# Performance work log

Measured on AMD Instinct MI355X. Metric: run time of the kernel, lower is better.

The kernel has to match this reference:

```python
import jax, jax.numpy as jnp
import numpy as np

B = 16384          # batch_size
NF = 50            # n_fields
K = 16             # embedding_dim
V = 1_000_000      # input_dim (vocab)
H = 400            # fc hidden
NNZ = B * NF


def _xavier(key, shape):
    fan_in, fan_out = shape
    lim = (6.0 / (fan_in + fan_out)) ** 0.5
    return jax.random.uniform(key, shape, minval=-lim, maxval=lim, dtype=jnp.float32)


def setup_inputs() -> dict:
    key = jax.random.key(0)
    ks = jax.random.split(key, 12)
    feats = jax.random.randint(ks[0], (NNZ,), 0, V)
    # n_fields contiguous features per sample (required by view(batch_size,-1))
    index = jnp.repeat(jnp.arange(B), NF)
    values = jax.random.uniform(ks[1], (NNZ,), dtype=jnp.float32)
    bias = jnp.zeros((1, 1), jnp.float32)
    weights = _xavier(ks[2], (V, 1))
    embedding = _xavier(ks[3], (V, K))
    d = NF * K  # 800
    W0 = _xavier(ks[4], (d, H))
    b0 = jax.random.normal(ks[5], (1, 1), jnp.float32)
    W1 = _xavier(ks[6], (H, H))
    b1 = jax.random.normal(ks[7], (1, 1), jnp.float32)
    W2 = _xavier(ks[8], (H, 1))
    b2 = jax.random.normal(ks[9], (1, 1), jnp.float32)
    return dict(index=index, feats=feats, values=values, bias=bias,
                weights=weights, embedding=embedding,
                W0=W0, b0=b0, W1=W1, b1=b1, W2=W2, b2=b2, batch_size=B)


def reference(index, feats, values, bias, weights, embedding,
              W0, b0, W1, b1, W2, b2, batch_size):
    # gather (F.embedding)
    w = weights[feats, 0]              # [nnz]
    emb = embedding[feats]             # [nnz, K]

    # first order: segment-sum of w*v, plus bias ([B] + [1,1] -> [1,B], as in torch)
    first = jax.ops.segment_sum(w * values, index, num_segments=batch_size) + bias

    # second order: FM pooling trick, fused over all K dims in one segment reduce
    ev = emb * values[:, None]                                        # [nnz, K]
    s1 = jax.ops.segment_sum(ev, index, num_segments=batch_size)      # [B, K]
    s2 = jax.ops.segment_sum(ev * ev, index, num_segments=batch_size) # [B, K]
    second = 0.5 * jnp.sum(s1 * s1 - s2, axis=1)                      # [B]

    # higher order MLP (relu on every layer, scalar biases)
    x = emb.reshape(batch_size, -1)    # [B, NF*K]
    x = jax.nn.relu(x @ W0 + b0)
    x = jax.nn.relu(x @ W1 + b1)
    x = jax.nn.relu(x @ W2 + b2)       # [B, 1]
    higher = x.reshape(-1)             # [B]

    return jax.nn.sigmoid(first + second + higher)  # [1, B]
```

## Files before the change

kernel.cpp:

```cpp
#include <hip/hip_runtime.h>
#include <hip/hip_bf16.h>


#define BATCH 16384
#define NFLD  50
#define EK    16
#define DDIM  800
#define HDIM  400
#define HPAD  416
#define NPAD  512

#define TB_W0 400
#define TB_W1 208
#define TBLK  (TB_W0 + TB_W1)
#define GBLK  (BATCH / 16)

typedef __attribute__((ext_vector_type(8))) __bf16 bf16x8;
typedef __attribute__((ext_vector_type(4))) float  f32x4;

typedef const __attribute__((address_space(1))) unsigned int* gas_u32p;
typedef __attribute__((address_space(3))) unsigned int*       las_u32p;

__device__ __forceinline__ void gld_lds16(const void* g, void* l) {
    __builtin_amdgcn_global_load_lds((gas_u32p)g, (las_u32p)l, 16, 0, 0);
}

__global__ __launch_bounds__(256) void prep_kernel(
    const float* __restrict__ W0, const float* __restrict__ W1,
    __hip_bfloat16* __restrict__ W0t, __hip_bfloat16* __restrict__ W1t,
    const int* __restrict__ feats, const float* __restrict__ values,
    const float* __restrict__ biasp, const float* __restrict__ weights,
    const float* __restrict__ embedding,
    float* __restrict__ fs, __hip_bfloat16* __restrict__ x)
{
    const int bid = blockIdx.x;
    if (bid < TBLK) {
        const int which = bid >= TB_W0;
        const int i  = which ? bid - TB_W0 : bid;
        const int nx = which ? 13 : 25;
        const int bx = i % nx, by = i / nx;
        const float* src = which ? W1 : W0;
        __hip_bfloat16* dst = which ? W1t : W0t;
        const int srcK = which ? HDIM : DDIM;
        const int dstCols = which ? HPAD : DDIM;

        __shared__ float tile[32][33];
        const int tx = threadIdx.x & 31, ty = threadIdx.x >> 5;
        const int k0 = bx * 32, n0 = by * 32;
#pragma unroll
        for (int r = 0; r < 4; ++r) {
            int k = k0 + ty + r * 8;
            int n = n0 + tx;
            float v = (k < srcK && n < HDIM) ? src[(long)k * HDIM + n] : 0.f;
            tile[ty + r * 8][tx] = v;
        }
        __syncthreads();
#pragma unroll
        for (int r = 0; r < 4; ++r) {
            int n = n0 + ty + r * 8;
            int k = k0 + tx;
            if (k < dstCols)
                dst[(long)n * dstCols + k] = __float2bfloat16(tile[tx][ty + r * 8]);
        }
        return;
    }

    const int wave = threadIdx.x >> 6;
    const int lane = threadIdx.x & 63;
    const int r    = lane >> 2, c = lane & 3;
    const int sbase = (bid - TBLK) * 16 + wave * 4;

    int   f[4] = {0, 0, 0, 0};
    float v[4] = {0.f, 0.f, 0.f, 0.f};
    float wsum[4] = {0.f, 0.f, 0.f, 0.f};
#pragma unroll
    for (int q = 0; q < 4; ++q) {
        const long base = (long)(sbase + q) * NFLD;
        if (lane < NFLD) {
            f[q] = feats[base + lane];
            v[q] = values[base + lane];
            wsum[q] = weights[f[q]] * v[q];
        }
    }

    int   fj[4][4]; float vj[4][4];
#pragma unroll
    for (int q = 0; q < 4; ++q)
#pragma unroll
        for (int p = 0; p < 4; ++p) {
            const int j = p * 16 + r;
            if (p < 3 || r < 2) {
                fj[q][p] = __shfl(f[q], j);
                vj[q][p] = __shfl(v[q], j);
            }
        }
    float4 e[4][4];
#pragma unroll
    for (int q = 0; q < 4; ++q)
#pragma unroll
        for (int p = 0; p < 4; ++p)
            if (p < 3 || r < 2)
                e[q][p] = *(const float4*)(embedding + (long)fj[q][p] * EK + c * 4);

#pragma unroll
    for (int q = 0; q < 4; ++q) {
        const int s = sbase + q;
        f32x4 s1 = {0.f, 0.f, 0.f, 0.f}, s2 = {0.f, 0.f, 0.f, 0.f};
#pragma unroll
        for (int p = 0; p < 4; ++p) {
            const int j = p * 16 + r;
            if (p < 3 || r < 2) {
                f32x4 ef = {e[q][p].x, e[q][p].y, e[q][p].z, e[q][p].w};
                f32x4 ev = ef * vj[q][p];
                s1 += ev;
                s2 += ev * ev;
                __hip_bfloat16 pk[4] = {
                    __float2bfloat16(e[q][p].x), __float2bfloat16(e[q][p].y),
                    __float2bfloat16(e[q][p].z), __float2bfloat16(e[q][p].w)};
                *(uint2*)&x[(long)s * DDIM + j * EK + c * 4] = *(uint2*)pk;
            }
        }
#pragma unroll
        for (int m = 4; m <= 32; m <<= 1) {
            s1.x += __shfl_xor(s1.x, m); s1.y += __shfl_xor(s1.y, m);
            s1.z += __shfl_xor(s1.z, m); s1.w += __shfl_xor(s1.w, m);
            s2.x += __shfl_xor(s2.x, m); s2.y += __shfl_xor(s2.y, m);
            s2.z += __shfl_xor(s2.z, m); s2.w += __shfl_xor(s2.w, m);
        }
        float t = (s1.x * s1.x - s2.x) + (s1.y * s1.y - s2.y)
                + (s1.z * s1.z - s2.z) + (s1.w * s1.w - s2.w);
        t += __shfl_xor(t, 1); t += __shfl_xor(t, 2);
        float w = wsum[q];
        w += __shfl_xor(w, 1);  w += __shfl_xor(w, 2);
        w += __shfl_xor(w, 4);  w += __shfl_xor(w, 8);
        w += __shfl_xor(w, 16); w += __shfl_xor(w, 32);
        if (lane == 0) fs[s] = w + 0.5f * t + biasp[0];
    }
}

#define OSTRIDE 136
template <int KDIM, int MODE, int LDC>
__global__ __launch_bounds__(256) void gemm_relu_kernel(
    const __hip_bfloat16* __restrict__ A,
    const __hip_bfloat16* __restrict__ Bt,
    const float* __restrict__ biasp,
    const float* __restrict__ W2,
    void* __restrict__ C)
{
    constexpr int KT = KDIM / 32;
    __shared__ __align__(16) char lds[128 * OSTRIDE * 2];
    __hip_bfloat16* sA = (__hip_bfloat16*)lds;
    __hip_bfloat16* sB = sA + 2 * 4096;
    __hip_bfloat16* sO = (__hip_bfloat16*)lds;

    const int tid  = threadIdx.x;
    const int wave = tid >> 6, lane = tid & 63;
    const int l16  = lane & 15, quad = lane >> 4;
    const int waveM = wave & 1, waveN = wave >> 1;
    const int m0 = blockIdx.y * 128;
    const int n0 = blockIdx.x * 128;

    f32x4 acc[4][4] = {};

    const long ar0 = (long)(m0 + wave * 16 + (lane >> 2)) * KDIM;
    const long ar1 = ar0 + (long)64 * KDIM;
    const long br0 = (long)(n0 + wave * 16 + (lane >> 2)) * KDIM;
    const long br1 = br0 + (long)64 * KDIM;
    const int  ac  = (lane & 3) * 8;
    __hip_bfloat16* ldsA0 = sA + wave * 512 + lane * 8;
    __hip_bfloat16* ldsA1 = sA + 2048 + wave * 512 + lane * 8;
    __hip_bfloat16* ldsB0 = sB + wave * 512 + lane * 8;
    __hip_bfloat16* ldsB1 = sB + 2048 + wave * 512 + lane * 8;

    auto stage = [&](int plane, int h) {
        const int k0 = plane * 32;
        gld_lds16(A  + ar0 + k0 + ac, ldsA0 + h * 4096);
        gld_lds16(A  + ar1 + k0 + ac, ldsA1 + h * 4096);
        gld_lds16(Bt + br0 + k0 + ac, ldsB0 + h * 4096);
        gld_lds16(Bt + br1 + k0 + ac, ldsB1 + h * 4096);
    };
    auto compute = [&](int h) {
        bf16x8 af[4], bfr[4];
#pragma unroll
        for (int i = 0; i < 4; ++i)
            af[i] = *(const bf16x8*)&sA[h * 4096 + (waveM * 64 + i * 16 + l16) * 32 + quad * 8];
#pragma unroll
        for (int j = 0; j < 4; ++j)
            bfr[j] = *(const bf16x8*)&sB[h * 4096 + (waveN * 64 + j * 16 + l16) * 32 + quad * 8];
#pragma unroll
        for (int i = 0; i < 4; ++i)
#pragma unroll
            for (int j = 0; j < 4; ++j)
                acc[i][j] = __builtin_amdgcn_mfma_f32_16x16x32_bf16(
                    af[i], bfr[j], acc[i][j], 0, 0, 0);
    };

    for (int kt = 0; kt + 1 < KT; kt += 2) {
        stage(kt, 0); stage(kt + 1, 1);
        __syncthreads();
        compute(0); compute(1);
        __syncthreads();
    }
    if constexpr (KT & 1) {
        stage(KT - 1, 0);
        __syncthreads();
        compute(0);
        __syncthreads();
    }

    const float bias = biasp[0];
    if constexpr (MODE == 0) {
#pragma unroll
        for (int i = 0; i < 4; ++i) {
            const int rl = waveM * 64 + i * 16 + quad * 4;
#pragma unroll
            for (int j = 0; j < 4; ++j) {
                const int cl = waveN * 64 + j * 16 + l16;
                const int gcol = n0 + cl;
#pragma unroll
                for (int r = 0; r < 4; ++r) {
                    float v = acc[i][j][r] + bias;
                    v = v > 0.f ? v : 0.f;
                    if (gcol >= HDIM) v = 0.f;
                    sO[(rl + r) * OSTRIDE + cl] = __float2bfloat16(v);
                }
            }
        }
        __syncthreads();
        __hip_bfloat16* Cp = (__hip_bfloat16*)C;
#pragma unroll
        for (int q = 0; q < 8; ++q) {
            const int flat = tid + q * 256;
            const int rl = flat >> 4, c16 = flat & 15;
            const int gcol = n0 + c16 * 8;
            if (gcol < LDC)
                *(float4*)&Cp[(long)(m0 + rl) * LDC + gcol] =
                    *(const float4*)&sO[rl * OSTRIDE + c16 * 8];
        }
    } else {
        float w2v[4];
#pragma unroll
        for (int j = 0; j < 4; ++j) {
            int col = n0 + waveN * 64 + j * 16 + l16;
            w2v[j] = (col < HDIM) ? W2[col] : 0.f;
        }
        const int slot = blockIdx.x * 2 + waveN;
#pragma unroll
        for (int i = 0; i < 4; ++i) {
#pragma unroll
            for (int r = 0; r < 4; ++r) {
                float p = 0.f;
#pragma unroll
                for (int j = 0; j < 4; ++j) {
                    float v = acc[i][j][r] + bias;
                    v = v > 0.f ? v : 0.f;
                    p += v * w2v[j];
                }
                p += __shfl_xor(p, 1); p += __shfl_xor(p, 2);
                p += __shfl_xor(p, 4); p += __shfl_xor(p, 8);
                if (l16 == 0) {
                    int row = m0 + waveM * 64 + i * 16 + quad * 4 + r;
                    ((float*)C)[(long)row * 8 + slot] = p;
                }
            }
        }
    }
}

__global__ __launch_bounds__(256) void final_kernel(
    const float* __restrict__ partial, const float* __restrict__ b2p,
    const float* __restrict__ fs, float* __restrict__ out)
{
    const int s = blockIdx.x * 256 + threadIdx.x;
    const float4 p0 = *(const float4*)(partial + (long)s * 8);
    const float4 p1 = *(const float4*)(partial + (long)s * 8 + 4);
    float sum = (p0.x + p0.y) + (p0.z + p0.w) + (p1.x + p1.y) + (p1.z + p1.w);
    float h = sum + b2p[0];
    h = h > 0.f ? h : 0.f;
    float z = fs[s] + h;
    out[s] = 1.f / (1.f + __expf(-z));
}

extern "C" void kernel_launch(void* const* d_in, const int* in_sizes, int n_in,
                              void* d_out, int out_size, void* d_ws, size_t ws_size,
                              hipStream_t stream)
{
    const int*   feats     = (const int*)d_in[1];
    const float* values    = (const float*)d_in[2];
    const float* bias      = (const float*)d_in[3];
    const float* weights   = (const float*)d_in[4];
    const float* embedding = (const float*)d_in[5];
    const float* W0 = (const float*)d_in[6];
    const float* b0 = (const float*)d_in[7];
    const float* W1 = (const float*)d_in[8];
    const float* b1 = (const float*)d_in[9];
    const float* W2 = (const float*)d_in[10];
    const float* b2 = (const float*)d_in[11];

    char* ws = (char*)d_ws;
    size_t off = 0;
    auto alloc = [&](size_t bytes) {
        void* p = ws + off;
        off += (bytes + 255) & ~(size_t)255;
        return p;
    };
    float*          fs   = (float*)alloc((size_t)BATCH * 4);
    __hip_bfloat16* x    = (__hip_bfloat16*)alloc((size_t)BATCH * DDIM * 2);
    __hip_bfloat16* h0   = (__hip_bfloat16*)alloc((size_t)BATCH * HPAD * 2);
    float*          part = (float*)alloc((size_t)BATCH * 8 * 4);
    __hip_bfloat16* W0t  = (__hip_bfloat16*)alloc((size_t)NPAD * DDIM * 2);
    __hip_bfloat16* W1t  = (__hip_bfloat16*)alloc((size_t)NPAD * HPAD * 2);
    (void)ws_size; (void)in_sizes; (void)n_in; (void)out_size;

    prep_kernel<<<dim3(TBLK + GBLK), 256, 0, stream>>>(
        W0, W1, W0t, W1t, feats, values, bias, weights, embedding, fs, x);
    gemm_relu_kernel<DDIM, 0, HPAD>
        <<<dim3(NPAD / 128, BATCH / 128), 256, 0, stream>>>(
        x, W0t, b0, nullptr, (void*)h0);
    gemm_relu_kernel<HPAD, 1, 8>
        <<<dim3(NPAD / 128, BATCH / 128), 256, 0, stream>>>(
        h0, W1t, b1, W2, (void*)part);
    final_kernel<<<dim3(BATCH / 256), 256, 0, stream>>>(
        part, b2, fs, (float*)d_out);
}
```

Baseline: 178.7 us.

## Fuse embedding gather, both MLP GEMMs and final sigmoid into one kernel

Replaces the separate GEMM kernels and the final kernel with a single fused kernel. Each block takes 64 rows, gathers embeddings directly from the table into registers as the A operand, keeps the first hidden layer in LDS, and runs the second GEMM plus the W2 dot product and sigmoid in place. This removes the global round trips for the bf16 x matrix, h0 and the partial sums, and drops two launches. In exchange it gathers A with scattered global loads inside the GEMM loop, each block covers all 448 columns, and LDS use is large enough to limit occupancy.

```diff
diff --git a/kernel.cpp b/kernel.cpp
--- a/kernel.cpp
+++ b/kernel.cpp
@@ -15,6 +15,15 @@
 #define TBLK  (TB_W0 + TB_W1)
 #define GBLK  (BATCH / 16)
 
+#define MROWS 64
+#define NCOLS 448
+#define WCOLS 112
+#define NFRAG 7
+#define P1    (DDIM / 32)
+#define P2    (HPAD / 32)
+#define H0S   424
+#define NCHUNK (NCOLS / 16)
+
 typedef __attribute__((ext_vector_type(8))) __bf16 bf16x8;
 typedef __attribute__((ext_vector_type(4))) float  f32x4;
 
@@ -23,6 +32,15 @@
 
 __device__ __forceinline__ void gld_lds16(const void* g, void* l) {
     __builtin_amdgcn_global_load_lds((gas_u32p)g, (las_u32p)l, 16, 0, 0);
+}
+
+__device__ __forceinline__ bf16x8 cvt8(const float4 a, const float4 b) {
+    union { __hip_bfloat16 h[8]; bf16x8 v; } u;
+    u.h[0] = __float2bfloat16(a.x); u.h[1] = __float2bfloat16(a.y);
+    u.h[2] = __float2bfloat16(a.z); u.h[3] = __float2bfloat16(a.w);
+    u.h[4] = __float2bfloat16(b.x); u.h[5] = __float2bfloat16(b.y);
+    u.h[6] = __float2bfloat16(b.z); u.h[7] = __float2bfloat16(b.w);
+    return u.v;
 }
 
 __global__ __launch_bounds__(256) void prep_kernel(
@@ -30,8 +48,7 @@
     __hip_bfloat16* __restrict__ W0t, __hip_bfloat16* __restrict__ W1t,
     const int* __restrict__ feats, const float* __restrict__ values,
     const float* __restrict__ biasp, const float* __restrict__ weights,
-    const float* __restrict__ embedding,
-    float* __restrict__ fs, __hip_bfloat16* __restrict__ x)
+    const float* __restrict__ embedding, float* __restrict__ fs)
 {
     const int bid = blockIdx.x;
     if (bid < TBLK) {
@@ -114,10 +131,6 @@
                 f32x4 ev = ef * vj[q][p];
                 s1 += ev;
                 s2 += ev * ev;
-                __hip_bfloat16 pk[4] = {
-                    __float2bfloat16(e[q][p].x), __float2bfloat16(e[q][p].y),
-                    __float2bfloat16(e[q][p].z), __float2bfloat16(e[q][p].w)};
-                *(uint2*)&x[(long)s * DDIM + j * EK + c * 4] = *(uint2*)pk;
             }
         }
 #pragma unroll
@@ -138,147 +151,165 @@
     }
 }
 
-#define OSTRIDE 136
-template <int KDIM, int MODE, int LDC>
-__global__ __launch_bounds__(256) void gemm_relu_kernel(
-    const __hip_bfloat16* __restrict__ A,
-    const __hip_bfloat16* __restrict__ Bt,
-    const float* __restrict__ biasp,
-    const float* __restrict__ W2,
-    void* __restrict__ C)
+__global__ __launch_bounds__(512, 2) void fused_mlp_kernel(
+    const int* __restrict__ feats, const float* __restrict__ embedding,
+    const __hip_bfloat16* __restrict__ W0t, const __hip_bfloat16* __restrict__ W1t,
+    const float* __restrict__ b0p, const float* __restrict__ b1p,
+    const float* __restrict__ W2, const float* __restrict__ b2p,
+    const float* __restrict__ fs, float* __restrict__ out)
 {
-    constexpr int KT = KDIM / 32;
-    __shared__ __align__(16) char lds[128 * OSTRIDE * 2];
-    __hip_bfloat16* sA = (__hip_bfloat16*)lds;
-    __hip_bfloat16* sB = sA + 2 * 4096;
-    __hip_bfloat16* sO = (__hip_bfloat16*)lds;
+    __shared__ __align__(16) __hip_bfloat16 sB[2][NCOLS * 32];
+    __shared__ __align__(16) __hip_bfloat16 h0p[MROWS * H0S];
+    __shared__ int   sfeat[MROWS * NFLD];
+    __shared__ float red[MROWS][4];
 
     const int tid  = threadIdx.x;
     const int wave = tid >> 6, lane = tid & 63;
     const int l16  = lane & 15, quad = lane >> 4;
     const int waveM = wave & 1, waveN = wave >> 1;
-    const int m0 = blockIdx.y * 128;
-    const int n0 = blockIdx.x * 128;
-
-    f32x4 acc[4][4] = {};
-
-    const long ar0 = (long)(m0 + wave * 16 + (lane >> 2)) * KDIM;
-    const long ar1 = ar0 + (long)64 * KDIM;
-    const long br0 = (long)(n0 + wave * 16 + (lane >> 2)) * KDIM;
-    const long br1 = br0 + (long)64 * KDIM;
-    const int  ac  = (lane & 3) * 8;
-    __hip_bfloat16* ldsA0 = sA + wave * 512 + lane * 8;
-    __hip_bfloat16* ldsA1 = sA + 2048 + wave * 512 + lane * 8;
-    __hip_bfloat16* ldsB0 = sB + wave * 512 + lane * 8;
-    __hip_bfloat16* ldsB1 = sB + 2048 + wave * 512 + lane * 8;
-
-    auto stage = [&](int plane, int h) {
-        const int k0 = plane * 32;
-        gld_lds16(A  + ar0 + k0 + ac, ldsA0 + h * 4096);
-        gld_lds16(A  + ar1 + k0 + ac, ldsA1 + h * 4096);
-        gld_lds16(Bt + br0 + k0 + ac, ldsB0 + h * 4096);
-        gld_lds16(Bt + br1 + k0 + ac, ldsB1 + h * 4096);
+    const int m0 = blockIdx.x * MROWS;
+
+    for (int i = tid; i < MROWS * NFLD; i += 512)
+        sfeat[i] = feats[(long)m0 * NFLD + i];
+
+    const float b0 = b0p[0];
+    const float b1 = b1p[0];
+
+    auto stageB = [&](const __hip_bfloat16* Bt, int ldb, int k0, int h) {
+#pragma unroll
+        for (int c = 0; c < 4; ++c) {
+            const int ch = wave + c * 8;
+            if (ch < NCHUNK) {
+                const __hip_bfloat16* src =
+                    Bt + (long)(ch * 16 + (lane >> 2)) * ldb + k0 + (lane & 3) * 8;
+                gld_lds16(src, &sB[h][ch * 512 + lane * 8]);
+            }
+        }
     };
-    auto compute = [&](int h) {
-        bf16x8 af[4], bfr[4];
-#pragma unroll
-        for (int i = 0; i < 4; ++i)
-            af[i] = *(const bf16x8*)&sA[h * 4096 + (waveM * 64 + i * 16 + l16) * 32 + quad * 8];
-#pragma unroll
-        for (int j = 0; j < 4; ++j)
-            bfr[j] = *(const bf16x8*)&sB[h * 4096 + (waveN * 64 + j * 16 + l16) * 32 + quad * 8];
-#pragma unroll
-        for (int i = 0; i < 4; ++i)
-#pragma unroll
-            for (int j = 0; j < 4; ++j)
+
+    auto loadA = [&](int p, float4* rg) {
+        const int f  = p * 2 + (quad >> 1);
+        const int d0 = (quad & 1) * 8;
+#pragma unroll
+        for (int i = 0; i < 2; ++i) {
+            const int row = waveM * 32 + i * 16 + l16;
+            const long fi = sfeat[row * NFLD + f];
+            const float* ep = embedding + fi * EK + d0;
+            rg[2 * i]     = *(const float4*)ep;
+            rg[2 * i + 1] = *(const float4*)(ep + 4);
+        }
+    };
+
+    f32x4 acc[2][NFRAG] = {};
+
+    __syncthreads();
+    float4 ra[4];
+    loadA(0, ra);
+    stageB(W0t, DDIM, 0, 0);
+    __syncthreads();
+
+#pragma unroll
+    for (int p = 0; p < P1; ++p) {
+        const int h = p & 1;
+        float4 rn[4];
+        if (p + 1 < P1) {
+            stageB(W0t, DDIM, (p + 1) * 32, h ^ 1);
+            loadA(p + 1, rn);
+        }
+        bf16x8 af[2];
+        af[0] = cvt8(ra[0], ra[1]);
+        af[1] = cvt8(ra[2], ra[3]);
+        bf16x8 bfr[NFRAG];
+#pragma unroll
+        for (int j = 0; j < NFRAG; ++j)
+            bfr[j] = *(const bf16x8*)&sB[h][(waveN * WCOLS + j * 16 + l16) * 32 + quad * 8];
+#pragma unroll
+        for (int i = 0; i < 2; ++i)
+#pragma unroll
+            for (int j = 0; j < NFRAG; ++j)
                 acc[i][j] = __builtin_amdgcn_mfma_f32_16x16x32_bf16(
                     af[i], bfr[j], acc[i][j], 0, 0, 0);
-    };
-
-    for (int kt = 0; kt + 1 < KT; kt += 2) {
-        stage(kt, 0); stage(kt + 1, 1);
         __syncthreads();
-        compute(0); compute(1);
+        if (p + 1 < P1) {
+#pragma unroll
+            for (int q = 0; q < 4; ++q) ra[q] = rn[q];
+        }
+    }
+
+#pragma unroll
+    for (int i = 0; i < 2; ++i)
+#pragma unroll
+        for (int j = 0; j < NFRAG; ++j) {
+            const int col = waveN * WCOLS + j * 16 + l16;
+            if (col < HPAD) {
+#pragma unroll
+                for (int r = 0; r < 4; ++r) {
+                    const int row = waveM * 32 + i * 16 + quad * 4 + r;
+                    float v = acc[i][j][r] + b0;
+                    v = v > 0.f ? v : 0.f;
+                    if (col >= HDIM) v = 0.f;
+                    h0p[row * H0S + col] = __float2bfloat16(v);
+                }
+            }
+        }
+
+    f32x4 acc2[2][NFRAG] = {};
+    stageB(W1t, HPAD, 0, 0);
+    float w2v[NFRAG];
+#pragma unroll
+    for (int j = 0; j < NFRAG; ++j) {
+        const int col = waveN * WCOLS + j * 16 + l16;
+        w2v[j] = (col < HDIM) ? W2[col] : 0.f;
+    }
+    __syncthreads();
+
+#pragma unroll
+    for (int p = 0; p < P2; ++p) {
+        const int h = p & 1;
+        if (p + 1 < P2)
+            stageB(W1t, HPAD, (p + 1) * 32, h ^ 1);
+        bf16x8 af[2];
+#pragma unroll
+        for (int i = 0; i < 2; ++i)
+            af[i] = *(const bf16x8*)&h0p[(waveM * 32 + i * 16 + l16) * H0S + p * 32 + quad * 8];
+        bf16x8 bfr[NFRAG];
+#pragma unroll
+        for (int j = 0; j < NFRAG; ++j)
+            bfr[j] = *(const bf16x8*)&sB[h][(waveN * WCOLS + j * 16 + l16) * 32 + quad * 8];
+#pragma unroll
+        for (int i = 0; i < 2; ++i)
+#pragma unroll
+            for (int j = 0; j < NFRAG; ++j)
+                acc2[i][j] = __builtin_amdgcn_mfma_f32_16x16x32_bf16(
+                    af[i], bfr[j], acc2[i][j], 0, 0, 0);
         __syncthreads();
     }
-    if constexpr (KT & 1) {
-        stage(KT - 1, 0);
-        __syncthreads();
-        compute(0);
-        __syncthreads();
-    }
-
-    const float bias = biasp[0];
-    if constexpr (MODE == 0) {
-#pragma unroll
-        for (int i = 0; i < 4; ++i) {
-            const int rl = waveM * 64 + i * 16 + quad * 4;
-#pragma unroll
-            for (int j = 0; j < 4; ++j) {
-                const int cl = waveN * 64 + j * 16 + l16;
-                const int gcol = n0 + cl;
-#pragma unroll
-                for (int r = 0; r < 4; ++r) {
-                    float v = acc[i][j][r] + bias;
-                    v = v > 0.f ? v : 0.f;
-                    if (gcol >= HDIM) v = 0.f;
-                    sO[(rl + r) * OSTRIDE + cl] = __float2bfloat16(v);
-                }
-            }
-        }
-        __syncthreads();
-        __hip_bfloat16* Cp = (__hip_bfloat16*)C;
-#pragma unroll
-        for (int q = 0; q < 8; ++q) {
-            const int flat = tid + q * 256;
-            const int rl = flat >> 4, c16 = flat & 15;
-            const int gcol = n0 + c16 * 8;
-            if (gcol < LDC)
-                *(float4*)&Cp[(long)(m0 + rl) * LDC + gcol] =
-                    *(const float4*)&sO[rl * OSTRIDE + c16 * 8];
-        }
-    } else {
-        float w2v[4];
-#pragma unroll
-        for (int j = 0; j < 4; ++j) {
-            int col = n0 + waveN * 64 + j * 16 + l16;
-            w2v[j] = (col < HDIM) ? W2[col] : 0.f;
-        }
-        const int slot = blockIdx.x * 2 + waveN;
-#pragma unroll
-        for (int i = 0; i < 4; ++i) {
-#pragma unroll
-            for (int r = 0; r < 4; ++r) {
-                float p = 0.f;
-#pragma unroll
-                for (int j = 0; j < 4; ++j) {
-                    float v = acc[i][j][r] + bias;
-                    v = v > 0.f ? v : 0.f;
-                    p += v * w2v[j];
-                }
-                p += __shfl_xor(p, 1); p += __shfl_xor(p, 2);
-                p += __shfl_xor(p, 4); p += __shfl_xor(p, 8);
-                if (l16 == 0) {
-                    int row = m0 + waveM * 64 + i * 16 + quad * 4 + r;
-                    ((float*)C)[(long)row * 8 + slot] = p;
-                }
-            }
-        }
-    }
-}
-
-__global__ __launch_bounds__(256) void final_kernel(
-    const float* __restrict__ partial, const float* __restrict__ b2p,
-    const float* __restrict__ fs, float* __restrict__ out)
-{
-    const int s = blockIdx.x * 256 + threadIdx.x;
-    const float4 p0 = *(const float4*)(partial + (long)s * 8);
-    const float4 p1 = *(const float4*)(partial + (long)s * 8 + 4);
-    float sum = (p0.x + p0.y) + (p0.z + p0.w) + (p1.x + p1.y) + (p1.z + p1.w);
-    float h = sum + b2p[0];
-    h = h > 0.f ? h : 0.f;
-    float z = fs[s] + h;
-    out[s] = 1.f / (1.f + __expf(-z));
+
+#pragma unroll
+    for (int i = 0; i < 2; ++i)
+#pragma unroll
+        for (int r = 0; r < 4; ++r) {
+            float ps = 0.f;
+#pragma unroll
+            for (int j = 0; j < NFRAG; ++j) {
+                float v = acc2[i][j][r] + b1;
+                v = v > 0.f ? v : 0.f;
+                ps += v * w2v[j];
+            }
+            ps += __shfl_xor(ps, 1); ps += __shfl_xor(ps, 2);
+            ps += __shfl_xor(ps, 4); ps += __shfl_xor(ps, 8);
+            if (l16 == 0)
+                red[waveM * 32 + i * 16 + quad * 4 + r][waveN] = ps;
+        }
+    __syncthreads();
+
+    if (tid < MROWS) {
+        const float s = (red[tid][0] + red[tid][1]) + (red[tid][2] + red[tid][3]);
+        float hv = s + b2p[0];
+        hv = hv > 0.f ? hv : 0.f;
+        const float z = fs[m0 + tid] + hv;
+        out[m0 + tid] = 1.f / (1.f + __expf(-z));
+    }
 }
 
 extern "C" void kernel_launch(void* const* d_in, const int* in_sizes, int n_in,
@@ -305,21 +336,12 @@
         return p;
     };
     float*          fs   = (float*)alloc((size_t)BATCH * 4);
-    __hip_bfloat16* x    = (__hip_bfloat16*)alloc((size_t)BATCH * DDIM * 2);
-    __hip_bfloat16* h0   = (__hip_bfloat16*)alloc((size_t)BATCH * HPAD * 2);
-    float*          part = (float*)alloc((size_t)BATCH * 8 * 4);
     __hip_bfloat16* W0t  = (__hip_bfloat16*)alloc((size_t)NPAD * DDIM * 2);
     __hip_bfloat16* W1t  = (__hip_bfloat16*)alloc((size_t)NPAD * HPAD * 2);
     (void)ws_size; (void)in_sizes; (void)n_in; (void)out_size;
 
     prep_kernel<<<dim3(TBLK + GBLK), 256, 0, stream>>>(
-        W0, W1, W0t, W1t, feats, values, bias, weights, embedding, fs, x);
-    gemm_relu_kernel<DDIM, 0, HPAD>
-        <<<dim3(NPAD / 128, BATCH / 128), 256, 0, stream>>>(
-        x, W0t, b0, nullptr, (void*)h0);
-    gemm_relu_kernel<HPAD, 1, 8>
-        <<<dim3(NPAD / 128, BATCH / 128), 256, 0, stream>>>(
-        h0, W1t, b1, W2, (void*)part);
-    final_kernel<<<dim3(BATCH / 256), 256, 0, stream>>>(
-        part, b2, fs, (float*)d_out);
-}
+        W0, W1, W0t, W1t, feats, values, bias, weights, embedding, fs);
+    fused_mlp_kernel<<<dim3(BATCH / MROWS), 512, 0, stream>>>(
+        feats, embedding, W0t, W1t, b0, b1, W2, b2, fs, (float*)d_out);
+}
```

Measured after the change: 187.1 us. +4.7%, slower.
